# Performance work log

Measured on AMD Instinct MI355X. Metric: run time of the kernel, lower is better.

Reference implementation:

```python
import jax, jax.numpy as jnp
import numpy as np

EMBED_DIM = 1024
NUM_HEADS = 16
HEAD_DIM = EMBED_DIM // NUM_HEADS
BATCH = 1
SEQ = 4096


def setup_inputs() -> dict:
    key = jax.random.key(0)
    ks = jax.random.split(key, 9)
    s = 1.0 / np.sqrt(EMBED_DIM)
    inp = {
        "x": jax.random.normal(ks[0], (BATCH, SEQ, EMBED_DIM), dtype=jnp.float32),
        "Wq": jax.random.uniform(ks[1], (EMBED_DIM, EMBED_DIM), jnp.float32, -s, s),
        "bq": jax.random.uniform(ks[2], (EMBED_DIM,), jnp.float32, -s, s),
        "Wk": jax.random.uniform(ks[3], (EMBED_DIM, EMBED_DIM), jnp.float32, -s, s),
        "bk": jax.random.uniform(ks[4], (EMBED_DIM,), jnp.float32, -s, s),
        "Wv": jax.random.uniform(ks[5], (EMBED_DIM, EMBED_DIM), jnp.float32, -s, s),
        "bv": jax.random.uniform(ks[6], (EMBED_DIM,), jnp.float32, -s, s),
        "Wo": jax.random.uniform(ks[7], (EMBED_DIM, EMBED_DIM), jnp.float32, -s, s),
        "bo": jax.random.uniform(ks[8], (EMBED_DIM,), jnp.float32, -s, s),
    }
    return inp


def _attention(x, Wq, bq, Wk, bk, Wv, bv, Wo, bo):
    B, S, E = x.shape
    # project and split heads: [B, H, S, D]
    def split_heads(t):
        return t.reshape(B, S, NUM_HEADS, HEAD_DIM).transpose(0, 2, 1, 3)
    q = split_heads(x @ Wq + bq)
    k = split_heads(x @ Wk + bk)
    v = split_heads(x @ Wv + bv)
    scale = 1.0 / np.sqrt(HEAD_DIM).astype(np.float32)
    # scores: [B, H, S, S] (torch code materializes these per query chunk;
    # math is identical computed in one shot)
    scores = jnp.einsum("bhqd,bhkd->bhqk", q, k) * scale
    attn = jax.nn.softmax(scores, axis=-1)  # dropout p=0 -> identity
    out = jnp.einsum("bhqk,bhkd->bhqd", attn, v)
    out = out.transpose(0, 2, 1, 3).reshape(B, S, E)
    return out @ Wo + bo


def reference(x, Wq, bq, Wk, bk, Wv, bv, Wo, bo):
    return _attention(x, Wq, bq, Wk, bk, Wv, bv, Wo, bo)
```

## Files before the change

### kernel.cpp

```cpp
#include <hip/hip_runtime.h>
#include <stdint.h>

typedef __bf16 bf16;
typedef __bf16 bf16x8 __attribute__((ext_vector_type(8)));
typedef float f32x4 __attribute__((ext_vector_type(4)));

#define EMB 1024
#define SEQ 4096
#define NH 16
#define HD 64

__device__ __forceinline__ void glds16(const void* g, void* l) {
    __builtin_amdgcn_global_load_lds(
        (const __attribute__((address_space(1))) uint32_t*)(uintptr_t)g,
        (__attribute__((address_space(3))) uint32_t*)(uintptr_t)l,
        16, 0, 0);
}

__global__ __launch_bounds__(256) void xcast_k(const float* __restrict__ in,
                                               bf16* __restrict__ out) {
    size_t base = ((size_t)blockIdx.x * 256 + threadIdx.x) * 16;
#pragma unroll
    for (int h = 0; h < 2; ++h) {
        f32x4 a = *(const f32x4*)(in + base + h * 8);
        f32x4 b = *(const f32x4*)(in + base + h * 8 + 4);
        bf16x8 v;
#pragma unroll
        for (int i = 0; i < 4; ++i) { v[i] = (bf16)a[i]; v[4 + i] = (bf16)b[i]; }
        *(bf16x8*)(out + base + h * 8) = v;
    }
}

__device__ __forceinline__ void transpose_body(const float* in, bf16* out,
                                               int R, int C) {
    __shared__ bf16 tile[64][81];
    const int t = threadIdx.x;
    const int rbase = blockIdx.y * 64;
    const int cbase = blockIdx.x * 64;
#pragma unroll
    for (int p = 0; p < 2; ++p) {
        int idx = t + p * 256;
        int r = idx >> 3;
        int seg = idx & 7;
        const float* src = in + (size_t)(rbase + r) * C + cbase + seg * 8;
        f32x4 a = *(const f32x4*)src;
        f32x4 b = *(const f32x4*)(src + 4);
#pragma unroll
        for (int i = 0; i < 4; ++i) {
            tile[r][seg * 8 + i]     = (bf16)a[i];
            tile[r][seg * 8 + 4 + i] = (bf16)b[i];
        }
    }
    __syncthreads();
#pragma unroll
    for (int p = 0; p < 2; ++p) {
        int idx = t + p * 256;
        int r = idx >> 3;
        int seg = idx & 7;
        bf16x8 v;
#pragma unroll
        for (int i = 0; i < 8; ++i) v[i] = tile[seg * 8 + i][r];
        *(bf16x8*)(out + (size_t)(cbase + r) * R + rbase + seg * 8) = v;
    }
}

__global__ __launch_bounds__(256) void transpose_k(const float* __restrict__ in,
                                                   bf16* __restrict__ out,
                                                   int R, int C) {
    transpose_body(in, out, R, C);
}

__global__ __launch_bounds__(256) void transpose3_k(const float* __restrict__ W0,
                                                    const float* __restrict__ W1,
                                                    const float* __restrict__ W2,
                                                    bf16* __restrict__ o0,
                                                    bf16* __restrict__ o1,
                                                    bf16* __restrict__ o2) {
    const float* in = blockIdx.z == 0 ? W0 : (blockIdx.z == 1 ? W1 : W2);
    bf16* out = blockIdx.z == 0 ? o0 : (blockIdx.z == 1 ? o1 : o2);
    transpose_body(in, out, EMB, EMB);
}

template<bool A_BF16, bool FUSED>
__global__ __launch_bounds__(256, 3) void gemm_m97(
    const void* __restrict__ A,
    const bf16* __restrict__ Wt0, const bf16* __restrict__ Wt1,
    const bf16* __restrict__ Wt2,
    const float* __restrict__ b0, const float* __restrict__ b1,
    const float* __restrict__ b2,
    void* __restrict__ out0, void* __restrict__ out1,
    bf16* __restrict__ outVt) {
    constexpr int SMEM_BYTES = A_BF16 ? (FUSED ? 18432 : 16384) : 24576;
    __shared__ __align__(16) uint8_t smem[SMEM_BYTES];
    float* aF = (float*)smem;
    bf16*  aB = (bf16*)smem;
    bf16*  bL = (bf16*)(smem + (A_BF16 ? 8192 : 16384));

    const int t = threadIdx.x;
    const int lane = t & 63;
    const int wave = t >> 6;
    const int l15 = lane & 15;
    const int quad = lane >> 4;
    const int wrow = (wave >> 1) * 64;
    const int wcol = (wave & 1) * 64;
    const int nb = blockIdx.x;
    const int which = FUSED ? (nb >> 3) : 0;
    const int ncol = (FUSED ? (nb & 7) : nb) * 128;
    const int mblock = blockIdx.y * 128;

    const bf16* Wt = FUSED ? (which == 0 ? Wt0 : (which == 1 ? Wt1 : Wt2)) : Wt0;
    const float* bias = FUSED ? (which == 0 ? b0 : (which == 1 ? b1 : b2)) : b0;

    float bv[4];
#pragma unroll
    for (int nt = 0; nt < 4; ++nt) bv[nt] = bias[ncol + wcol + nt * 16 + l15];

    f32x4 acc[4][4];
#pragma unroll
    for (int mt = 0; mt < 4; ++mt)
#pragma unroll
        for (int nt = 0; nt < 4; ++nt) acc[mt][nt] = (f32x4){0.f, 0.f, 0.f, 0.f};

    const int a4row = lane >> 3, a4seg = lane & 7;
    const int b2row = lane >> 2, b2seg = lane & 3;

    for (int k0 = 0; k0 < EMB; k0 += 32) {
        __syncthreads();
        if constexpr (!A_BF16) {
#pragma unroll
            for (int i = 0; i < 4; ++i) {
                int row = i * 32 + wave * 8 + a4row;
                int sg = a4seg ^ (row & 7);
                glds16((const float*)A + (size_t)(mblock + row) * EMB + k0 + sg * 4,
                       smem + i * 4096 + wave * 1024);
            }
        } else {
#pragma unroll
            for (int i = 0; i < 2; ++i) {
                int row = i * 64 + wave * 16 + b2row;
                int sg = b2seg ^ ((row >> 1) & 3);
                glds16((const bf16*)A + (size_t)(mblock + row) * EMB + k0 + sg * 8,
                       smem + i * 4096 + wave * 1024);
            }
        }
#pragma unroll
        for (int i = 0; i < 2; ++i) {
            int row = i * 64 + wave * 16 + b2row;
            int sg = b2seg ^ ((row >> 1) & 3);
            glds16(Wt + (size_t)(ncol + row) * EMB + k0 + sg * 8,
                   (uint8_t*)bL + i * 4096 + wave * 1024);
        }
        __syncthreads();

        bf16x8 af[4], bfr[4];
#pragma unroll
        for (int mt = 0; mt < 4; ++mt) {
            int rl = wrow + mt * 16 + l15;
            if constexpr (!A_BF16) {
                f32x4 lo = *(const f32x4*)(aF + rl * 32 + ((2 * quad)     ^ (rl & 7)) * 4);
                f32x4 hi = *(const f32x4*)(aF + rl * 32 + ((2 * quad + 1) ^ (rl & 7)) * 4);
#pragma unroll
                for (int j = 0; j < 4; ++j) {
                    af[mt][j]     = (bf16)lo[j];
                    af[mt][4 + j] = (bf16)hi[j];
                }
            } else {
                af[mt] = *(const bf16x8*)(aB + rl * 32 + (quad ^ ((rl >> 1) & 3)) * 8);
            }
        }
#pragma unroll
        for (int nt = 0; nt < 4; ++nt) {
            int rl = wcol + nt * 16 + l15;
            bfr[nt] = *(const bf16x8*)(bL + rl * 32 + (quad ^ ((rl >> 1) & 3)) * 8);
        }
#pragma unroll
        for (int mt = 0; mt < 4; ++mt)
#pragma unroll
            for (int nt = 0; nt < 4; ++nt)
                acc[mt][nt] = __builtin_amdgcn_mfma_f32_16x16x32_bf16(
                    af[mt], bfr[nt], acc[mt][nt], 0, 0, 0);
    }

    if (!FUSED || which < 2) {
        void* outp = FUSED ? (which == 0 ? out0 : out1) : out0;
#pragma unroll
        for (int mt = 0; mt < 4; ++mt)
#pragma unroll
            for (int nt = 0; nt < 4; ++nt)
#pragma unroll
                for (int r = 0; r < 4; ++r) {
                    size_t row = mblock + wrow + mt * 16 + quad * 4 + r;
                    size_t col = ncol + wcol + nt * 16 + l15;
                    float v = acc[mt][nt][r] + bv[nt];
                    if constexpr (FUSED) ((bf16*)outp)[row * EMB + col] = (bf16)v;
                    else                 ((float*)outp)[row * EMB + col] = v;
                }
    } else if constexpr (FUSED) {
        __syncthreads();
        bf16* tr = (bf16*)smem + wave * 2304;
#pragma unroll
        for (int ch = 0; ch < 2; ++ch) {
#pragma unroll
            for (int mt = 0; mt < 4; ++mt)
#pragma unroll
                for (int ntl = 0; ntl < 2; ++ntl)
#pragma unroll
                    for (int r = 0; r < 4; ++r) {
                        int d_local = ntl * 16 + l15;
                        int s_local = mt * 16 + quad * 4 + r;
                        int nt = 2 * ch + ntl;
                        tr[d_local * 72 + s_local] = (bf16)(acc[mt][nt][r] + bv[nt]);
                    }
            int d2 = lane & 31, h2 = lane >> 5;
#pragma unroll
            for (int j = 0; j < 4; ++j) {
                bf16x8 v = *(const bf16x8*)(tr + d2 * 72 + h2 * 32 + j * 8);
                *(bf16x8*)(outVt + (size_t)(ncol + wcol + ch * 32 + d2) * SEQ +
                           mblock + wrow + h2 * 32 + j * 8) = v;
            }
        }
    }
}

__global__ __launch_bounds__(256, 2) void attn_k(bf16* __restrict__ QO,
                                                 const bf16* __restrict__ Km,
                                                 const bf16* __restrict__ Vt) {
    __shared__ bf16 k_lds[2][64 * 64];
    __shared__ bf16 v_lds[2][64 * 64];
    __shared__ bf16 p_lds[4][2][16][72];
    const int t = threadIdx.x;
    const int lane = t & 63;
    const int wave = t >> 6;
    const int l15 = lane & 15;
    const int quad = lane >> 4;
    const int sw = l15 & 7;
    const int h = blockIdx.y;
    const int qbase = blockIdx.x * 128 + wave * 32;
    const float QSCALE = 0.125f * 1.4426950408889634f;

    const int srow = wave * 16 + (lane >> 3);
    const int ssg  = lane & 7;

    bf16x8 qf[2][2];
#pragma unroll
    for (int qt = 0; qt < 2; ++qt)
#pragma unroll
        for (int kk = 0; kk < 2; ++kk) {
            bf16x8 raw = *(const bf16x8*)(QO + (size_t)(qbase + qt * 16 + l15) * EMB +
                                          h * HD + kk * 32 + quad * 8);
#pragma unroll
            for (int j = 0; j < 8; ++j) qf[qt][kk][j] = (bf16)((float)raw[j] * QSCALE);
        }

    f32x4 o_acc[2][4];
#pragma unroll
    for (int qt = 0; qt < 2; ++qt)
#pragma unroll
        for (int c = 0; c < 4; ++c) o_acc[qt][c] = (f32x4){0.f, 0.f, 0.f, 0.f};
    float l_run[2][4] = {{0.f, 0.f, 0.f, 0.f}, {0.f, 0.f, 0.f, 0.f}};

#define STAGE(buf, kbv)                                                               \
    do {                                                                              \
        _Pragma("unroll")                                                             \
        for (int i = 0; i < 2; ++i) {                                                 \
            int rr = srow + i * 8;                                                    \
            int sg = ssg ^ (rr & 7);                                                  \
            glds16(Km + (size_t)((kbv) + rr) * EMB + h * HD + sg * 8,                 \
                   &k_lds[buf][(wave * 16 + i * 8) * 64]);                            \
            glds16(Vt + (size_t)(h * HD + rr) * SEQ + (kbv) + sg * 8,                 \
                   &v_lds[buf][(wave * 16 + i * 8) * 64]);                            \
        }                                                                             \
    } while (0)

#define COMPUTE(buf)                                                                  \
    do {                                                                              \
        f32x4 s[2][4];                                                                \
        _Pragma("unroll")                                                             \
        for (int c = 0; c < 4; ++c) {                                                 \
            int row = c * 16 + l15;                                                   \
            bf16x8 k0 = *(const bf16x8*)&k_lds[buf][row * 64 + ((quad)     ^ sw) * 8];\
            bf16x8 k1 = *(const bf16x8*)&k_lds[buf][row * 64 + ((4 + quad) ^ sw) * 8];\
            _Pragma("unroll")                                                         \
            for (int qt = 0; qt < 2; ++qt) {                                          \
                f32x4 z = (f32x4){0.f, 0.f, 0.f, 0.f};                                \
                z = __builtin_amdgcn_mfma_f32_16x16x32_bf16(qf[qt][0], k0, z, 0, 0, 0);\
                s[qt][c] = __builtin_amdgcn_mfma_f32_16x16x32_bf16(qf[qt][1], k1, z, 0, 0, 0);\
            }                                                                         \
        }                                                                             \
        _Pragma("unroll")                                                             \
        for (int qt = 0; qt < 2; ++qt)                                                \
            _Pragma("unroll")                                                         \
            for (int r = 0; r < 4; ++r)                                               \
                _Pragma("unroll")                                                     \
                for (int c = 0; c < 4; ++c) {                                         \
                    float p = __builtin_amdgcn_exp2f(s[qt][c][r]);                    \
                    l_run[qt][r] += p;                                                \
                    p_lds[wave][qt][quad * 4 + r][c * 16 + l15] = (bf16)p;            \
                }                                                                     \
        bf16x8 pf[2][2];                                                              \
        _Pragma("unroll")                                                             \
        for (int qt = 0; qt < 2; ++qt)                                                \
            _Pragma("unroll")                                                         \
            for (int tt = 0; tt < 2; ++tt)                                            \
                pf[qt][tt] = *(const bf16x8*)&p_lds[wave][qt][l15][tt * 32 + quad * 8];\
        _Pragma("unroll")                                                             \
        for (int c = 0; c < 4; ++c) {                                                 \
            int row = c * 16 + l15;                                                   \
            bf16x8 v0 = *(const bf16x8*)&v_lds[buf][row * 64 + ((quad)     ^ sw) * 8];\
            bf16x8 v1 = *(const bf16x8*)&v_lds[buf][row * 64 + ((4 + quad) ^ sw) * 8];\
            _Pragma("unroll")                                                         \
            for (int qt = 0; qt < 2; ++qt) {                                          \
                o_acc[qt][c] = __builtin_amdgcn_mfma_f32_16x16x32_bf16(               \
                    pf[qt][0], v0, o_acc[qt][c], 0, 0, 0);                            \
                o_acc[qt][c] = __builtin_amdgcn_mfma_f32_16x16x32_bf16(               \
                    pf[qt][1], v1, o_acc[qt][c], 0, 0, 0);                            \
            }                                                                         \
        }                                                                             \
    } while (0)

    STAGE(0, 0);
    for (int kb = 0; kb < SEQ; kb += 128) {
        __syncthreads();
        STAGE(1, kb + 64);
        COMPUTE(0);
        __syncthreads();
        if (kb + 128 < SEQ) STAGE(0, kb + 128);
        COMPUTE(1);
    }
#undef STAGE
#undef COMPUTE

#pragma unroll
    for (int qt = 0; qt < 2; ++qt)
#pragma unroll
        for (int r = 0; r < 4; ++r) {
            float l = l_run[qt][r];
#pragma unroll
            for (int off = 1; off < 16; off <<= 1) l += __shfl_xor(l, off);
            float inv = 1.0f / l;
#pragma unroll
            for (int c = 0; c < 4; ++c)
                QO[(size_t)(qbase + qt * 16 + quad * 4 + r) * EMB + h * HD + c * 16 + l15] =
                    (bf16)(o_acc[qt][c][r] * inv);
        }
}

extern "C" void kernel_launch(void* const* d_in, const int* in_sizes, int n_in,
                              void* d_out, int out_size, void* d_ws, size_t ws_size,
                              hipStream_t stream) {
    const float* x  = (const float*)d_in[0];
    const float* Wq = (const float*)d_in[1];
    const float* bq = (const float*)d_in[2];
    const float* Wk = (const float*)d_in[3];
    const float* bk = (const float*)d_in[4];
    const float* Wv = (const float*)d_in[5];
    const float* bv = (const float*)d_in[6];
    const float* Wo = (const float*)d_in[7];
    const float* bo = (const float*)d_in[8];

    const size_t MAT = (size_t)SEQ * EMB;
    const size_t WMT = (size_t)EMB * EMB;

    bf16* o16   = (bf16*)d_out;
    bf16* Wt_q  = o16;
    bf16* Wt_k  = o16 + WMT;
    bf16* Wt_v  = o16 + 2 * WMT;
    bf16* Vtb   = o16 + 3 * WMT;

    bf16* wsb   = (bf16*)d_ws;
    bf16* QOb   = wsb;
    bf16* Kb    = wsb + MAT;
    bf16* Wt_o  = wsb + MAT;
    bf16* xb    = wsb + 2 * MAT;

    dim3 blk(256);
    dim3 gT3(EMB / 64, EMB / 64, 3);
    dim3 gTW(EMB / 64, EMB / 64);
    dim3 gF(24, SEQ / 128);
    dim3 gO(EMB / 128, SEQ / 128);
    dim3 gA(SEQ / 128, NH);

    transpose3_k<<<gT3, blk, 0, stream>>>(Wq, Wk, Wv, Wt_q, Wt_k, Wt_v);

    if (ws_size >= 3 * MAT * sizeof(bf16)) {
        xcast_k<<<dim3(MAT / (256 * 16)), blk, 0, stream>>>(x, xb);
        gemm_m97<true, true><<<gF, blk, 0, stream>>>(
            xb, Wt_q, Wt_k, Wt_v, bq, bk, bv, QOb, Kb, Vtb);
    } else {
        gemm_m97<false, true><<<gF, blk, 0, stream>>>(
            x, Wt_q, Wt_k, Wt_v, bq, bk, bv, QOb, Kb, Vtb);
    }

    attn_k<<<gA, blk, 0, stream>>>(QOb, Kb, Vtb);

    transpose_k<<<gTW, blk, 0, stream>>>(Wo, Wt_o, EMB, EMB);
    gemm_m97<true, false><<<gO, blk, 0, stream>>>(
        QOb, Wt_o, nullptr, nullptr, bo, nullptr, nullptr, d_out, nullptr, nullptr);
}
```

Measured before the change: 246.8 us.

## Fuse weight transposes and x cast into fewer kernel launches

The separate x-cast and QKV weight-transpose kernels are merged into one prep kernel, with z-slice 3 doing the cast. The Wo transpose moves into extra blocks of the attention kernel (blockIdx.y == NH), writing into the now-free xb buffer. This removes two kernel launches and the inter-kernel gaps, and overlaps the Wo transpose with attention. The trade-off is one extra row of blocks in the attention grid, and the fallback path now uses three separate transpose launches.

```diff
diff --git a/kernel.cpp b/kernel.cpp
--- a/kernel.cpp
+++ b/kernel.cpp
@@ -17,26 +17,10 @@
         16, 0, 0);
 }
 
-__global__ __launch_bounds__(256) void xcast_k(const float* __restrict__ in,
-                                               bf16* __restrict__ out) {
-    size_t base = ((size_t)blockIdx.x * 256 + threadIdx.x) * 16;
-#pragma unroll
-    for (int h = 0; h < 2; ++h) {
-        f32x4 a = *(const f32x4*)(in + base + h * 8);
-        f32x4 b = *(const f32x4*)(in + base + h * 8 + 4);
-        bf16x8 v;
-#pragma unroll
-        for (int i = 0; i < 4; ++i) { v[i] = (bf16)a[i]; v[4 + i] = (bf16)b[i]; }
-        *(bf16x8*)(out + base + h * 8) = v;
-    }
-}
-
-__device__ __forceinline__ void transpose_body(const float* in, bf16* out,
-                                               int R, int C) {
-    __shared__ bf16 tile[64][81];
+__device__ __forceinline__ void transpose_tile(const float* in, bf16* out,
+                                               int R, int C, int rbase, int cbase,
+                                               bf16* tile ) {
     const int t = threadIdx.x;
-    const int rbase = blockIdx.y * 64;
-    const int cbase = blockIdx.x * 64;
 #pragma unroll
     for (int p = 0; p < 2; ++p) {
         int idx = t + p * 256;
@@ -47,8 +31,8 @@
         f32x4 b = *(const f32x4*)(src + 4);
 #pragma unroll
         for (int i = 0; i < 4; ++i) {
-            tile[r][seg * 8 + i]     = (bf16)a[i];
-            tile[r][seg * 8 + 4 + i] = (bf16)b[i];
+            tile[r * 81 + seg * 8 + i]     = (bf16)a[i];
+            tile[r * 81 + seg * 8 + 4 + i] = (bf16)b[i];
         }
     }
     __syncthreads();
@@ -59,26 +43,47 @@
         int seg = idx & 7;
         bf16x8 v;
 #pragma unroll
-        for (int i = 0; i < 8; ++i) v[i] = tile[seg * 8 + i][r];
+        for (int i = 0; i < 8; ++i) v[i] = tile[(seg * 8 + i) * 81 + r];
         *(bf16x8*)(out + (size_t)(cbase + r) * R + rbase + seg * 8) = v;
+    }
+}
+
+__global__ __launch_bounds__(256) void prep_k(const float* __restrict__ W0,
+                                              const float* __restrict__ W1,
+                                              const float* __restrict__ W2,
+                                              bf16* __restrict__ o0,
+                                              bf16* __restrict__ o1,
+                                              bf16* __restrict__ o2,
+                                              const float* __restrict__ x,
+                                              bf16* __restrict__ xb) {
+    __shared__ bf16 tile[64 * 81];
+    if (blockIdx.z < 3) {
+        const float* in = blockIdx.z == 0 ? W0 : (blockIdx.z == 1 ? W1 : W2);
+        bf16* out = blockIdx.z == 0 ? o0 : (blockIdx.z == 1 ? o1 : o2);
+        transpose_tile(in, out, EMB, EMB, blockIdx.y * 64, blockIdx.x * 64, tile);
+    } else {
+        size_t linear = blockIdx.y * 16 + blockIdx.x;
+#pragma unroll
+        for (int i = 0; i < 4; ++i) {
+            size_t base = linear * 16384 + (size_t)i * 4096 + threadIdx.x * 16;
+#pragma unroll
+            for (int h = 0; h < 2; ++h) {
+                f32x4 a = *(const f32x4*)(x + base + h * 8);
+                f32x4 b = *(const f32x4*)(x + base + h * 8 + 4);
+                bf16x8 v;
+#pragma unroll
+                for (int j = 0; j < 4; ++j) { v[j] = (bf16)a[j]; v[4 + j] = (bf16)b[j]; }
+                *(bf16x8*)(xb + base + h * 8) = v;
+            }
+        }
     }
 }
 
 __global__ __launch_bounds__(256) void transpose_k(const float* __restrict__ in,
                                                    bf16* __restrict__ out,
                                                    int R, int C) {
-    transpose_body(in, out, R, C);
-}
-
-__global__ __launch_bounds__(256) void transpose3_k(const float* __restrict__ W0,
-                                                    const float* __restrict__ W1,
-                                                    const float* __restrict__ W2,
-                                                    bf16* __restrict__ o0,
-                                                    bf16* __restrict__ o1,
-                                                    bf16* __restrict__ o2) {
-    const float* in = blockIdx.z == 0 ? W0 : (blockIdx.z == 1 ? W1 : W2);
-    bf16* out = blockIdx.z == 0 ? o0 : (blockIdx.z == 1 ? o1 : o2);
-    transpose_body(in, out, EMB, EMB);
+    __shared__ bf16 tile[64 * 81];
+    transpose_tile(in, out, R, C, blockIdx.y * 64, blockIdx.x * 64, tile);
 }
 
 template<bool A_BF16, bool FUSED>
@@ -224,10 +229,25 @@
 
 __global__ __launch_bounds__(256, 2) void attn_k(bf16* __restrict__ QO,
                                                  const bf16* __restrict__ Km,
-                                                 const bf16* __restrict__ Vt) {
+                                                 const bf16* __restrict__ Vt,
+                                                 const float* __restrict__ Wo,
+                                                 bf16* __restrict__ wt_o) {
     __shared__ bf16 k_lds[2][64 * 64];
     __shared__ bf16 v_lds[2][64 * 64];
     __shared__ bf16 p_lds[4][2][16][72];
+
+    if (blockIdx.y == NH) {
+        bf16* tile = &k_lds[0][0];
+#pragma unroll 1
+        for (int i = 0; i < 8; ++i) {
+            int tid = blockIdx.x * 8 + i;
+            int ty = tid >> 4, tx = tid & 15;
+            transpose_tile(Wo, wt_o, EMB, EMB, ty * 64, tx * 64, tile);
+            __syncthreads();
+        }
+        return;
+    }
+
     const int t = threadIdx.x;
     const int lane = t & 63;
     const int wave = t >> 6;
@@ -370,30 +390,36 @@
     bf16* wsb   = (bf16*)d_ws;
     bf16* QOb   = wsb;
     bf16* Kb    = wsb + MAT;
-    bf16* Wt_o  = wsb + MAT;
     bf16* xb    = wsb + 2 * MAT;
 
     dim3 blk(256);
-    dim3 gT3(EMB / 64, EMB / 64, 3);
-    dim3 gTW(EMB / 64, EMB / 64);
+    dim3 gP(16, 16, 4);
     dim3 gF(24, SEQ / 128);
     dim3 gO(EMB / 128, SEQ / 128);
-    dim3 gA(SEQ / 128, NH);
-
-    transpose3_k<<<gT3, blk, 0, stream>>>(Wq, Wk, Wv, Wt_q, Wt_k, Wt_v);
 
     if (ws_size >= 3 * MAT * sizeof(bf16)) {
-        xcast_k<<<dim3(MAT / (256 * 16)), blk, 0, stream>>>(x, xb);
+        prep_k<<<gP, blk, 0, stream>>>(Wq, Wk, Wv, Wt_q, Wt_k, Wt_v, x, xb);
+
         gemm_m97<true, true><<<gF, blk, 0, stream>>>(
             xb, Wt_q, Wt_k, Wt_v, bq, bk, bv, QOb, Kb, Vtb);
+
+        dim3 gA(SEQ / 128, NH + 1);
+        attn_k<<<gA, blk, 0, stream>>>(QOb, Kb, Vtb, Wo, xb);
+
+        gemm_m97<true, false><<<gO, blk, 0, stream>>>(
+            QOb, xb, nullptr, nullptr, bo, nullptr, nullptr, d_out, nullptr, nullptr);
     } else {
+        bf16* Wt_o = wsb + MAT;
+        dim3 gTW(EMB / 64, EMB / 64);
+        transpose_k<<<gTW, blk, 0, stream>>>(Wq, Wt_q, EMB, EMB);
+        transpose_k<<<gTW, blk, 0, stream>>>(Wk, Wt_k, EMB, EMB);
+        transpose_k<<<gTW, blk, 0, stream>>>(Wv, Wt_v, EMB, EMB);
         gemm_m97<false, true><<<gF, blk, 0, stream>>>(
             x, Wt_q, Wt_k, Wt_v, bq, bk, bv, QOb, Kb, Vtb);
-    }
-
-    attn_k<<<gA, blk, 0, stream>>>(QOb, Kb, Vtb);
-
-    transpose_k<<<gTW, blk, 0, stream>>>(Wo, Wt_o, EMB, EMB);
-    gemm_m97<true, false><<<gO, blk, 0, stream>>>(
-        QOb, Wt_o, nullptr, nullptr, bo, nullptr, nullptr, d_out, nullptr, nullptr);
-}
+        dim3 gA(SEQ / 128, NH);
+        attn_k<<<gA, blk, 0, stream>>>(QOb, Kb, Vtb, nullptr, nullptr);
+        transpose_k<<<gTW, blk, 0, stream>>>(Wo, Wt_o, EMB, EMB);
+        gemm_m97<true, false><<<gO, blk, 0, stream>>>(
+            QOb, Wt_o, nullptr, nullptr, bo, nullptr, nullptr, d_out, nullptr, nullptr);
+    }
+}
```

Result: no change. 243.6 us (-1.3%).
